# Kernel optimization log

Measured on AMD Instinct MI355X. Metric: run time of the kernel, lower is better.

The kernel has to match this reference:

```python
import jax, jax.numpy as jnp
import numpy as np

B, K, D, C = 8192, 16, 1024, 512


def setup_inputs() -> dict:
    key = jax.random.key(0)
    k1, k2, k3, k4, k5 = jax.random.split(key, 5)
    concepts = jax.random.normal(k1, (B, K, D), dtype=jnp.float32)
    slot_ids = jax.random.randint(k2, (B,), 0, K)
    labels = jax.random.randint(k3, (B,), 0, C)
    # per-slot Linear(concept_dim -> num_classes): weight (K, C, D), bias (K, C)
    W = jax.random.normal(k4, (K, C, D), dtype=jnp.float32) / np.sqrt(D).astype(np.float32)
    bias = jax.random.normal(k5, (K, C), dtype=jnp.float32) * 0.01
    return {"concepts": concepts, "slot_ids": slot_ids, "labels": labels, "W": W, "bias": bias}


def reference(concepts, slot_ids, labels, W, bias):
    # Each example b uses slot s=slot_ids[b]: logits = concepts[b, s, :] @ W[s].T + bias[s].
    # Vectorized as K batched GEMMs over the slot axis, then gather the relevant row.
    logits = jnp.einsum('bkd,kcd->bkc', concepts, W) + bias  # (B, K, C)
    logp = jax.nn.log_softmax(logits, axis=-1)
    bidx = jnp.arange(concepts.shape[0])
    ce = -logp[bidx, slot_ids, labels]  # per-example cross entropy (B,)
    nK = W.shape[0]
    counts = jax.ops.segment_sum(jnp.ones_like(ce), slot_ids, num_segments=nK)
    sums = jax.ops.segment_sum(ce, slot_ids, num_segments=nK)
    means = sums / jnp.maximum(counts, 1.0)          # per-slot mean CE (= F.cross_entropy per group)
    present = counts > 0
    n_present = jnp.maximum(jnp.sum(present), 1)     # torch: count of unique slots, max(count,1)
    return jnp.sum(jnp.where(present, means, 0.0)) / n_present
```

## Files before the change

kernel.cpp:

```cpp
#include <hip/hip_runtime.h>
#include <hip/hip_bf16.h>

#define B_N 8192
#define K_N 16
#define D_N 1024
#define C_N 512
#define BM  32

typedef __bf16 bf16x8 __attribute__((ext_vector_type(8)));
typedef float  f32x4  __attribute__((ext_vector_type(4)));
typedef float  f32x4v __attribute__((ext_vector_type(4)));
typedef unsigned int u32x4 __attribute__((ext_vector_type(4)));
typedef unsigned int u32x2 __attribute__((ext_vector_type(2)));

static __device__ __forceinline__ unsigned short f2bf(float f) {
    union { float f; unsigned int u; } x; x.f = f;
    unsigned int r = x.u + 0x7FFFu + ((x.u >> 16) & 1u);
    return (unsigned short)(r >> 16);
}

static __device__ __forceinline__ bf16x8 load_bf8(const unsigned short* p) {
    union { u32x4 u; bf16x8 v; } t;
    t.u = *(const u32x4*)p;
    return t.v;
}

static __device__ __forceinline__ bf16x8 zero_bf8() {
    union { u32x4 u; bf16x8 v; } t;
    u32x4 z = {0u, 0u, 0u, 0u};
    t.u = z;
    return t.v;
}


__global__ void initk(int* counts, int* cursors, float* ce_sums) {
    int t = threadIdx.x;
    if (t < K_N) { counts[t] = 0; cursors[t] = 0; ce_sums[t] = 0.f; }
}

__global__ void countk(const int* __restrict__ slot_ids, int* __restrict__ counts) {
    __shared__ int h[K_N];
    if (threadIdx.x < K_N) h[threadIdx.x] = 0;
    __syncthreads();
    for (int b = blockIdx.x * blockDim.x + threadIdx.x; b < B_N; b += gridDim.x * blockDim.x)
        atomicAdd(&h[slot_ids[b]], 1);
    __syncthreads();
    if (threadIdx.x < K_N) atomicAdd(&counts[threadIdx.x], h[threadIdx.x]);
}

__global__ void scank(const int* __restrict__ counts, int* __restrict__ offsets) {
    if (threadIdx.x == 0 && blockIdx.x == 0) {
        int a = 0;
        for (int s = 0; s < K_N; ++s) { offsets[s] = a; a += counts[s]; }
    }
}

__global__ void scatterk(const int* __restrict__ slot_ids, const int* __restrict__ labels,
                         const int* __restrict__ offsets, int* __restrict__ cursors,
                         int* __restrict__ order_rows, int* __restrict__ lab_g) {
    for (int b = blockIdx.x * blockDim.x + threadIdx.x; b < B_N; b += gridDim.x * blockDim.x) {
        int s = slot_ids[b];
        int p = atomicAdd(&cursors[s], 1);
        int idx = offsets[s] + p;
        order_rows[idx] = b * K_N + s;
        lab_g[idx] = labels[b];
    }
}

__global__ void convw(const float* __restrict__ W, unsigned short* __restrict__ Wb) {
    int i = (blockIdx.x * 256 + threadIdx.x) * 8;
    f32x4v a = *(const f32x4v*)(W + i);
    f32x4v b = *(const f32x4v*)(W + i + 4);
    u32x4 o;
    o[0] = (unsigned)f2bf(a[0]) | ((unsigned)f2bf(a[1]) << 16);
    o[1] = (unsigned)f2bf(a[2]) | ((unsigned)f2bf(a[3]) << 16);
    o[2] = (unsigned)f2bf(b[0]) | ((unsigned)f2bf(b[1]) << 16);
    o[3] = (unsigned)f2bf(b[2]) | ((unsigned)f2bf(b[3]) << 16);
    *(u32x4*)(Wb + i) = o;
}

__global__ void gatherx(const float* __restrict__ concepts, const int* __restrict__ order_rows,
                        unsigned short* __restrict__ Xg) {
    int idx = blockIdx.x;
    int row = order_rows[idx];
    const float* in = concepts + (size_t)row * D_N;
    unsigned short* out = Xg + (size_t)idx * D_N;
    int t = threadIdx.x * 4;
    f32x4v a = *(const f32x4v*)(in + t);
    u32x2 o;
    o[0] = (unsigned)f2bf(a[0]) | ((unsigned)f2bf(a[1]) << 16);
    o[1] = (unsigned)f2bf(a[2]) | ((unsigned)f2bf(a[3]) << 16);
    *(u32x2*)(out + t) = o;
}

__global__ __launch_bounds__(256) void gemm_ce(
        const unsigned short* __restrict__ Xg, const unsigned short* __restrict__ Wb,
        const float* __restrict__ bias, const int* __restrict__ counts,
        const int* __restrict__ offsets, const int* __restrict__ lab_g,
        float* __restrict__ ce_sums) {
    int s = blockIdx.y;
    int cnt = counts[s];
    int row0 = blockIdx.x * BM;
    if (row0 >= cnt) return;
    int nrows = min(BM, cnt - row0);
    int base = offsets[s];

    int tid = threadIdx.x;
    int wave = tid >> 6, lane = tid & 63;
    int col = lane & 15, quad = lane >> 4;
    int c0 = wave * 128;

    f32x4 acc[2][8];
    f32x4 zf = {0.f, 0.f, 0.f, 0.f};
#pragma unroll
    for (int m = 0; m < 2; ++m)
#pragma unroll
        for (int t = 0; t < 8; ++t) acc[m][t] = zf;

    const unsigned short* aptr[2];
    bool avalid[2];
#pragma unroll
    for (int m = 0; m < 2; ++m) {
        int lr = m * 16 + col;
        avalid[m] = lr < nrows;
        int gr = base + row0 + (avalid[m] ? lr : 0);
        aptr[m] = Xg + (size_t)gr * D_N + quad * 8;
    }
    const unsigned short* bptr = Wb + ((size_t)s * C_N + c0 + col) * D_N + quad * 8;

    for (int k = 0; k < D_N; k += 32) {
        bf16x8 af[2];
#pragma unroll
        for (int m = 0; m < 2; ++m)
            af[m] = avalid[m] ? load_bf8(aptr[m] + k) : zero_bf8();
        bf16x8 bfr[8];
#pragma unroll
        for (int t = 0; t < 8; ++t)
            bfr[t] = load_bf8(bptr + (size_t)t * 16 * D_N + k);
#pragma unroll
        for (int m = 0; m < 2; ++m)
#pragma unroll
            for (int t = 0; t < 8; ++t)
                acc[m][t] = __builtin_amdgcn_mfma_f32_16x16x32_bf16(af[m], bfr[t], acc[m][t], 0, 0, 0);
    }

    __shared__ float smax[4][BM];
    __shared__ float ssum[4][BM];
    __shared__ float gmax[BM];
    __shared__ float slab[BM];

#pragma unroll
    for (int t = 0; t < 8; ++t) {
        float bv = bias[(size_t)s * C_N + c0 + t * 16 + col];
#pragma unroll
        for (int m = 0; m < 2; ++m)
#pragma unroll
            for (int r = 0; r < 4; ++r) acc[m][t][r] += bv;
    }

#pragma unroll
    for (int m = 0; m < 2; ++m)
#pragma unroll
        for (int r = 0; r < 4; ++r) {
            float v = acc[m][0][r];
#pragma unroll
            for (int t = 1; t < 8; ++t) v = fmaxf(v, acc[m][t][r]);
            v = fmaxf(v, __shfl_xor(v, 1, 64));
            v = fmaxf(v, __shfl_xor(v, 2, 64));
            v = fmaxf(v, __shfl_xor(v, 4, 64));
            v = fmaxf(v, __shfl_xor(v, 8, 64));
            if (col == 0) smax[wave][m * 16 + quad * 4 + r] = v;
        }
    __syncthreads();
    if (tid < BM)
        gmax[tid] = fmaxf(fmaxf(smax[0][tid], smax[1][tid]),
                          fmaxf(smax[2][tid], smax[3][tid]));
    __syncthreads();

#pragma unroll
    for (int m = 0; m < 2; ++m)
#pragma unroll
        for (int r = 0; r < 4; ++r) {
            int row = m * 16 + quad * 4 + r;
            float gm = gmax[row];
            int lab = (row < nrows) ? lab_g[base + row0 + row] : -1;
            float sv = 0.f;
#pragma unroll
            for (int t = 0; t < 8; ++t) {
                float x = acc[m][t][r];
                sv += __expf(x - gm);
                if (c0 + t * 16 + col == lab) slab[row] = x;
            }
            sv += __shfl_xor(sv, 1, 64);
            sv += __shfl_xor(sv, 2, 64);
            sv += __shfl_xor(sv, 4, 64);
            sv += __shfl_xor(sv, 8, 64);
            if (col == 0) ssum[wave][row] = sv;
        }
    __syncthreads();

    if (wave == 0) {
        float ce = 0.f;
        if (lane < nrows) {
            float gs = ssum[0][lane] + ssum[1][lane] + ssum[2][lane] + ssum[3][lane];
            ce = gmax[lane] + __logf(gs) - slab[lane];
        }
        ce += __shfl_xor(ce, 1, 64);
        ce += __shfl_xor(ce, 2, 64);
        ce += __shfl_xor(ce, 4, 64);
        ce += __shfl_xor(ce, 8, 64);
        ce += __shfl_xor(ce, 16, 64);
        ce += __shfl_xor(ce, 32, 64);
        if (lane == 0) atomicAdd(&ce_sums[s], ce);
    }
}

__global__ void finalize(const int* __restrict__ counts, const float* __restrict__ ce_sums,
                         float* __restrict__ out) {
    if (threadIdx.x == 0 && blockIdx.x == 0) {
        float tot = 0.f; int np = 0;
        for (int s = 0; s < K_N; ++s) {
            int c = counts[s];
            if (c > 0) { tot += ce_sums[s] / (float)c; np++; }
        }
        out[0] = tot / (float)(np > 0 ? np : 1);
    }
}

extern "C" void kernel_launch(void* const* d_in, const int* in_sizes, int n_in,
                              void* d_out, int out_size, void* d_ws, size_t ws_size,
                              hipStream_t stream) {
    const float* concepts = (const float*)d_in[0];
    const int*   slot_ids = (const int*)d_in[1];
    const int*   labels   = (const int*)d_in[2];
    const float* W        = (const float*)d_in[3];
    const float* bias     = (const float*)d_in[4];
    float* out = (float*)d_out;

    char* ws = (char*)d_ws;
    int*   counts     = (int*)(ws + 0);
    int*   offsets    = (int*)(ws + 64);
    int*   cursors    = (int*)(ws + 128);
    float* ce_sums    = (float*)(ws + 192);
    int*   order_rows = (int*)(ws + 256);
    int*   lab_g      = (int*)(ws + 256 + 4 * B_N);
    unsigned short* Wb = (unsigned short*)(ws + 131072);
    unsigned short* Xg = (unsigned short*)(ws + 131072 + (size_t)2 * K_N * C_N * D_N);

    initk<<<1, 64, 0, stream>>>(counts, cursors, ce_sums);
    countk<<<32, 256, 0, stream>>>(slot_ids, counts);
    scank<<<1, 1, 0, stream>>>(counts, offsets);
    scatterk<<<32, 256, 0, stream>>>(slot_ids, labels, offsets, cursors, order_rows, lab_g);
    convw<<<(K_N * C_N * D_N) / (256 * 8), 256, 0, stream>>>(W, Wb);
    gatherx<<<B_N, 256, 0, stream>>>(concepts, order_rows, Xg);
    gemm_ce<<<dim3(B_N / BM, K_N), 256, 0, stream>>>(Xg, Wb, bias, counts, offsets, lab_g, ce_sums);
    finalize<<<1, 1, 0, stream>>>(counts, ce_sums, out);
}
```

Baseline: 745.9 us.

## Fuse index prep into one kernel and gather fp32 rows directly in GEMM

Replaces the init/count/scan/scatter kernels with a single-block prep kernel that uses per-thread histograms and a shared-memory prefix scan, which removes launches and global atomics. It also drops the gatherx pass, so the GEMM reads fp32 concept rows straight through order_rows and converts them to bf16 in registers. This avoids writing and re-reading the bf16 Xg buffer. In exchange, the A-operand loads double in size, and a row is re-read by every block that uses it. The single-block prep serializes the index work.

```diff
diff --git a/kernel.cpp b/kernel.cpp
--- a/kernel.cpp
+++ b/kernel.cpp
@@ -11,7 +11,6 @@
 typedef float  f32x4  __attribute__((ext_vector_type(4)));
 typedef float  f32x4v __attribute__((ext_vector_type(4)));
 typedef unsigned int u32x4 __attribute__((ext_vector_type(4)));
-typedef unsigned int u32x2 __attribute__((ext_vector_type(2)));
 
 static __device__ __forceinline__ unsigned short f2bf(float f) {
     union { float f; unsigned int u; } x; x.f = f;
@@ -32,36 +31,68 @@
     return t.v;
 }
 
-
-__global__ void initk(int* counts, int* cursors, float* ce_sums) {
+__global__ __launch_bounds__(256) void prep(const int* __restrict__ slot_ids,
+                                            const int* __restrict__ labels,
+                                            int* __restrict__ counts,
+                                            int* __restrict__ offsets_g,
+                                            float* __restrict__ ce_sums,
+                                            int* __restrict__ order_rows,
+                                            int* __restrict__ lab_g) {
+    __shared__ int h[256][K_N];
+    __shared__ int g[256][K_N];
+    __shared__ int soff[K_N];
     int t = threadIdx.x;
-    if (t < K_N) { counts[t] = 0; cursors[t] = 0; ce_sums[t] = 0.f; }
-}
-
-__global__ void countk(const int* __restrict__ slot_ids, int* __restrict__ counts) {
-    __shared__ int h[K_N];
-    if (threadIdx.x < K_N) h[threadIdx.x] = 0;
-    __syncthreads();
-    for (int b = blockIdx.x * blockDim.x + threadIdx.x; b < B_N; b += gridDim.x * blockDim.x)
-        atomicAdd(&h[slot_ids[b]], 1);
-    __syncthreads();
-    if (threadIdx.x < K_N) atomicAdd(&counts[threadIdx.x], h[threadIdx.x]);
-}
-
-__global__ void scank(const int* __restrict__ counts, int* __restrict__ offsets) {
-    if (threadIdx.x == 0 && blockIdx.x == 0) {
+    int ids[32];
+
+#pragma unroll
+    for (int s = 0; s < K_N; ++s) h[t][s] = 0;
+#pragma unroll
+    for (int i = 0; i < 32; ++i) {
+        int b = i * 256 + t;
+        int s = slot_ids[b];
+        ids[i] = s;
+        h[t][s]++;
+    }
+#pragma unroll
+    for (int s = 0; s < K_N; ++s) g[t][s] = h[t][s];
+    __syncthreads();
+
+    for (int d = 1; d < 256; d <<= 1) {
+        int v[K_N];
+        if (t >= d) {
+#pragma unroll
+            for (int s = 0; s < K_N; ++s) v[s] = h[t - d][s];
+        }
+        __syncthreads();
+        if (t >= d) {
+#pragma unroll
+            for (int s = 0; s < K_N; ++s) h[t][s] += v[s];
+        }
+        __syncthreads();
+    }
+
+    if (t == 0) {
         int a = 0;
-        for (int s = 0; s < K_N; ++s) { offsets[s] = a; a += counts[s]; }
-    }
-}
-
-__global__ void scatterk(const int* __restrict__ slot_ids, const int* __restrict__ labels,
-                         const int* __restrict__ offsets, int* __restrict__ cursors,
-                         int* __restrict__ order_rows, int* __restrict__ lab_g) {
-    for (int b = blockIdx.x * blockDim.x + threadIdx.x; b < B_N; b += gridDim.x * blockDim.x) {
-        int s = slot_ids[b];
-        int p = atomicAdd(&cursors[s], 1);
-        int idx = offsets[s] + p;
+#pragma unroll
+        for (int s = 0; s < K_N; ++s) {
+            int c = h[255][s];
+            counts[s] = c;
+            soff[s] = a;
+            offsets_g[s] = a;
+            a += c;
+        }
+    }
+    if (t < K_N) ce_sums[t] = 0.f;
+    __syncthreads();
+
+#pragma unroll
+    for (int s = 0; s < K_N; ++s) h[t][s] = soff[s] + h[t][s] - g[t][s];
+
+#pragma unroll
+    for (int i = 0; i < 32; ++i) {
+        int b = i * 256 + t;
+        int s = ids[i];
+        int idx = h[t][s]++;
         order_rows[idx] = b * K_N + s;
         lab_g[idx] = labels[b];
     }
@@ -79,25 +110,11 @@
     *(u32x4*)(Wb + i) = o;
 }
 
-__global__ void gatherx(const float* __restrict__ concepts, const int* __restrict__ order_rows,
-                        unsigned short* __restrict__ Xg) {
-    int idx = blockIdx.x;
-    int row = order_rows[idx];
-    const float* in = concepts + (size_t)row * D_N;
-    unsigned short* out = Xg + (size_t)idx * D_N;
-    int t = threadIdx.x * 4;
-    f32x4v a = *(const f32x4v*)(in + t);
-    u32x2 o;
-    o[0] = (unsigned)f2bf(a[0]) | ((unsigned)f2bf(a[1]) << 16);
-    o[1] = (unsigned)f2bf(a[2]) | ((unsigned)f2bf(a[3]) << 16);
-    *(u32x2*)(out + t) = o;
-}
-
 __global__ __launch_bounds__(256) void gemm_ce(
-        const unsigned short* __restrict__ Xg, const unsigned short* __restrict__ Wb,
+        const float* __restrict__ concepts, const unsigned short* __restrict__ Wb,
         const float* __restrict__ bias, const int* __restrict__ counts,
-        const int* __restrict__ offsets, const int* __restrict__ lab_g,
-        float* __restrict__ ce_sums) {
+        const int* __restrict__ offsets, const int* __restrict__ order_rows,
+        const int* __restrict__ lab_g, float* __restrict__ ce_sums) {
     int s = blockIdx.y;
     int cnt = counts[s];
     int row0 = blockIdx.x * BM;
@@ -110,6 +127,11 @@
     int col = lane & 15, quad = lane >> 4;
     int c0 = wave * 128;
 
+    __shared__ int srow[BM];
+    if (tid < BM)
+        srow[tid] = order_rows[base + row0 + min(tid, nrows - 1)];
+    __syncthreads();
+
     f32x4 acc[2][8];
     f32x4 zf = {0.f, 0.f, 0.f, 0.f};
 #pragma unroll
@@ -117,22 +139,29 @@
 #pragma unroll
         for (int t = 0; t < 8; ++t) acc[m][t] = zf;
 
-    const unsigned short* aptr[2];
+    const float* aptr[2];
     bool avalid[2];
 #pragma unroll
     for (int m = 0; m < 2; ++m) {
         int lr = m * 16 + col;
         avalid[m] = lr < nrows;
-        int gr = base + row0 + (avalid[m] ? lr : 0);
-        aptr[m] = Xg + (size_t)gr * D_N + quad * 8;
+        aptr[m] = concepts + (size_t)srow[lr] * D_N + quad * 8;
     }
     const unsigned short* bptr = Wb + ((size_t)s * C_N + c0 + col) * D_N + quad * 8;
 
     for (int k = 0; k < D_N; k += 32) {
         bf16x8 af[2];
 #pragma unroll
-        for (int m = 0; m < 2; ++m)
-            af[m] = avalid[m] ? load_bf8(aptr[m] + k) : zero_bf8();
+        for (int m = 0; m < 2; ++m) {
+            f32x4 a0 = *(const f32x4*)(aptr[m] + k);
+            f32x4 a1 = *(const f32x4*)(aptr[m] + k + 4);
+            bf16x8 v;
+            v[0] = (__bf16)a0[0]; v[1] = (__bf16)a0[1];
+            v[2] = (__bf16)a0[2]; v[3] = (__bf16)a0[3];
+            v[4] = (__bf16)a1[0]; v[5] = (__bf16)a1[1];
+            v[6] = (__bf16)a1[2]; v[7] = (__bf16)a1[3];
+            af[m] = avalid[m] ? v : zero_bf8();
+        }
         bf16x8 bfr[8];
 #pragma unroll
         for (int t = 0; t < 8; ++t)
@@ -240,19 +269,14 @@
     char* ws = (char*)d_ws;
     int*   counts     = (int*)(ws + 0);
     int*   offsets    = (int*)(ws + 64);
-    int*   cursors    = (int*)(ws + 128);
     float* ce_sums    = (float*)(ws + 192);
     int*   order_rows = (int*)(ws + 256);
     int*   lab_g      = (int*)(ws + 256 + 4 * B_N);
     unsigned short* Wb = (unsigned short*)(ws + 131072);
-    unsigned short* Xg = (unsigned short*)(ws + 131072 + (size_t)2 * K_N * C_N * D_N);
-
-    initk<<<1, 64, 0, stream>>>(counts, cursors, ce_sums);
-    countk<<<32, 256, 0, stream>>>(slot_ids, counts);
-    scank<<<1, 1, 0, stream>>>(counts, offsets);
-    scatterk<<<32, 256, 0, stream>>>(slot_ids, labels, offsets, cursors, order_rows, lab_g);
+
     convw<<<(K_N * C_N * D_N) / (256 * 8), 256, 0, stream>>>(W, Wb);
-    gatherx<<<B_N, 256, 0, stream>>>(concepts, order_rows, Xg);
-    gemm_ce<<<dim3(B_N / BM, K_N), 256, 0, stream>>>(Xg, Wb, bias, counts, offsets, lab_g, ce_sums);
+    prep<<<1, 256, 0, stream>>>(slot_ids, labels, counts, offsets, ce_sums, order_rows, lab_g);
+    gemm_ce<<<dim3(B_N / BM, K_N), 256, 0, stream>>>(concepts, Wb, bias, counts, offsets,
+                                                     order_rows, lab_g, ce_sums);
     finalize<<<1, 1, 0, stream>>>(counts, ce_sums, out);
 }
```

New measurement: 750.6 us. Within noise of the previous version (+0.6%).
